# Performance work log

Measured on AMD Instinct MI355X. Metric: run time of the kernel, lower is better.

Reference implementation:

```python
import math
import jax, jax.numpy as jnp
import numpy as np

N_HEAD = 16
D_MODEL = 1024
D_K = 64
D_V = 64


def setup_inputs() -> dict:
    key = jax.random.key(0)
    ks = jax.random.split(key, 9)
    bs, s = 8, 1024
    q = jax.random.normal(ks[0], (bs, s, D_K), dtype=jnp.float32)
    k = jax.random.normal(ks[1], (bs, s, D_K), dtype=jnp.float32)
    v = jax.random.normal(ks[2], (bs, s, D_V), dtype=jnp.float32)
    # NOTE: the source module only ever uses linear_q (applied to q, k, v alike),
    # so we only materialize that projection. Torch Linear: y = x @ W.T + b.
    Wq = jax.random.normal(ks[3], (N_HEAD * D_K, D_K), dtype=jnp.float32) * 0.02
    bq = jnp.zeros((N_HEAD * D_K,), dtype=jnp.float32)
    W1 = jax.random.normal(ks[4], (D_MODEL, N_HEAD * D_V), dtype=jnp.float32) * 0.02
    b1 = jnp.zeros((D_MODEL,), dtype=jnp.float32)
    W2 = jax.random.normal(ks[5], (D_MODEL, D_MODEL), dtype=jnp.float32) * 0.02
    b2 = jnp.zeros((D_MODEL,), dtype=jnp.float32)
    return {"q": q, "k": k, "v": v, "Wq": Wq, "bq": bq,
            "W1": W1, "b1": b1, "W2": W2, "b2": b2}


def reference(q, k, v, Wq, bq, W1, b1, W2, b2):
    bs, s_q, d_k = q.shape
    h = N_HEAD
    scale = math.sqrt(d_k)
    # shared projection (source uses linear_q for all three); split heads on last dim
    proj = lambda x: (jnp.einsum('bsd,ed->bse', x, Wq) + bq).reshape(bs, -1, h, d_k)
    qh = proj(q)   # [b, s_q, h, d]
    kh = proj(k)   # [b, s_k, h, d]
    vh = proj(v)   # [b, s_v, h, d]
    e = jnp.einsum('bqhd,bkhd->bhqk', qh, kh) / scale
    a = jax.nn.softmax(e, axis=-1)  # dropout = identity in eval mode
    y = jnp.einsum('bhqk,bkhd->bqhd', a, vh).reshape(bs, s_q, h * d_k)
    # output MLP: Linear -> ReLU -> (dropout) -> Linear
    x = jax.nn.relu(jnp.einsum('bsd,ed->bse', y, W1) + b1)
    x = jnp.einsum('bsd,ed->bse', x, W2) + b2
    return x
```

## Files before the change

### kernel.cpp

```cpp
#include <hip/hip_runtime.h>
#include <math.h>

#define NB 8
#define SS 1024
#define NH 16
#define DK 64
#define EE 1024
#define DMOD 1024

using bf16x8 = __attribute__((ext_vector_type(8))) short;
using f32x4  = __attribute__((ext_vector_type(4))) float;

__device__ __forceinline__ unsigned short f2bf(float f) {
    unsigned u = __builtin_bit_cast(unsigned, f);
    u += 0x7FFFu + ((u >> 16) & 1u);
    return (unsigned short)(u >> 16);
}

__device__ __forceinline__ float exp2_hw(float x) {
#if __has_builtin(__builtin_amdgcn_exp2f)
    return __builtin_amdgcn_exp2f(x);
#else
    float r; asm("v_exp_f32 %0, %1" : "=v"(r) : "v"(x)); return r;
#endif
}

__device__ __forceinline__ unsigned cvt_pk_bf16(float lo, float hi) {
    unsigned r;
    asm("v_cvt_pk_bf16_f32 %0, %1, %2" : "=v"(r) : "v"(lo), "v"(hi));
    return r;
}

__device__ __forceinline__ void gld16(const void* g, void* l) {
    __builtin_amdgcn_global_load_lds(
        (const __attribute__((address_space(1))) void*)g,
        (__attribute__((address_space(3))) void*)l, 16, 0, 0);
}

__global__ __launch_bounds__(256) void cvt_all(
    const float* __restrict__ W1, const float* __restrict__ W2,
    const float* __restrict__ q, const float* __restrict__ k,
    const float* __restrict__ v, const float* __restrict__ Wq,
    unsigned short* __restrict__ W1b, unsigned short* __restrict__ W2b,
    unsigned short* __restrict__ qb, unsigned short* __restrict__ kb,
    unsigned short* __restrict__ vb, unsigned short* __restrict__ Wqb)
{
    const int z = blockIdx.y;
    const float* s; unsigned short* d; int n;
    switch (z) {
        case 0:  s = W1; d = W1b; n = 1048576; break;
        case 1:  s = W2; d = W2b; n = 1048576; break;
        case 2:  s = q;  d = qb;  n = 524288;  break;
        case 3:  s = k;  d = kb;  n = 524288;  break;
        case 4:  s = v;  d = vb;  n = 524288;  break;
        default: s = Wq; d = Wqb; n = 65536;   break;
    }
    const int i = (blockIdx.x * 256 + threadIdx.x) * 8;
    if (i >= n) return;
    const float4 a = *(const float4*)(s + i);
    const float4 b = *(const float4*)(s + i + 4);
    bf16x8 o;
    o[0]=(short)f2bf(a.x); o[1]=(short)f2bf(a.y); o[2]=(short)f2bf(a.z); o[3]=(short)f2bf(a.w);
    o[4]=(short)f2bf(b.x); o[5]=(short)f2bf(b.y); o[6]=(short)f2bf(b.z); o[7]=(short)f2bf(b.w);
    *(bf16x8*)(d + i) = o;
}

__global__ __launch_bounds__(256) void proj_mfma(
    const unsigned short* __restrict__ qb, const unsigned short* __restrict__ kb,
    const unsigned short* __restrict__ vb, const unsigned short* __restrict__ Wb,
    const float* __restrict__ bias, unsigned short* __restrict__ Cbase,
    float qscale)
{
    __shared__ __align__(16) unsigned short As[128 * 64];
    __shared__ __align__(16) unsigned short Bs[128 * 64];
    const int z = blockIdx.z;
    const unsigned short* X = (z == 0) ? qb : (z == 1) ? kb : vb;
    unsigned short* C = Cbase + (size_t)z * 8388608;
    const float sc = (z == 0) ? qscale : 1.0f;
    const int tid  = threadIdx.x;
    const int lane = tid & 63;
    const int w = tid >> 6, wm = w >> 1, wn = w & 1;
    const int n0 = blockIdx.x * 128, m0 = blockIdx.y * 128;
    const int lr = lane & 15, lg = lane >> 4;

    #pragma unroll
    for (int p = 0; p < 4; ++p) {
        const int c = p * 256 + tid;
        const int lb = (p * 256 + (tid & ~63)) * 8;
        gld16(X  + (size_t)m0 * DK + (size_t)c * 8, As + lb);
        gld16(Wb + (size_t)n0 * DK + (size_t)c * 8, Bs + lb);
    }
    __syncthreads();

    f32x4 acc[4][4] = {};
    #pragma unroll
    for (int kk = 0; kk < 2; ++kk) {
        bf16x8 af[4], bfr[4];
        #pragma unroll
        for (int mf = 0; mf < 4; ++mf)
            af[mf] = *(const bf16x8*)&As[(wm * 64 + mf * 16 + lr) * 64 + kk * 32 + lg * 8];
        #pragma unroll
        for (int nf = 0; nf < 4; ++nf)
            bfr[nf] = *(const bf16x8*)&Bs[(wn * 64 + nf * 16 + lr) * 64 + kk * 32 + lg * 8];
        #pragma unroll
        for (int mf = 0; mf < 4; ++mf)
            #pragma unroll
            for (int nf = 0; nf < 4; ++nf)
                acc[mf][nf] = __builtin_amdgcn_mfma_f32_16x16x32_bf16(
                    af[mf], bfr[nf], acc[mf][nf], 0, 0, 0);
    }

    #pragma unroll
    for (int nf = 0; nf < 4; ++nf) {
        const int n = n0 + wn * 64 + nf * 16 + lr;
        const float bb = bias[n];
        #pragma unroll
        for (int mf = 0; mf < 4; ++mf)
            #pragma unroll
            for (int r = 0; r < 4; ++r) {
                const int mr = m0 + wm * 64 + mf * 16 + lg * 4 + r;
                const int bh = (mr >> 10) * NH + (n >> 6);
                const int s  = mr & 1023, d = n & 63;
                const size_t idx = (z == 2)
                    ? (size_t)bh * 65536 + (size_t)d * 1024 + s
                    : (size_t)bh * 65536 + (size_t)s * 64 + d;
                C[idx] = f2bf((acc[mf][nf][r] + bb) * sc);
            }
    }
}

__global__ __launch_bounds__(256) void attn_v9(
    const unsigned short* __restrict__ Qp, const unsigned short* __restrict__ Kp,
    const unsigned short* __restrict__ Vt, unsigned short* __restrict__ Y)
{
    __shared__ __align__(16) unsigned short Ks[64 * 64];
    __shared__ __align__(16) unsigned short Vs[64 * 64];
    __shared__ __align__(16) unsigned short Ps[4][32][72];
    const int tid  = threadIdx.x;
    const int lane = tid & 63;
    const int w    = tid >> 6;
    const int flat    = blockIdx.x;
    const int logical = (flat & 7) * 128 + (flat >> 3);
    const int qt = logical & 7;
    const int bh = logical >> 3;
    const int q0 = qt * 128;
    const size_t base = (size_t)bh * (SS * DK);
    const int lr = lane & 15, lg = lane >> 4;
    const int lg4 = lg * 4;

    const int c0 = tid,       r0 = c0 >> 3, h0 = c0 & 7;
    const int c1 = 256 + tid, r1 = c1 >> 3, h1 = c1 & 7;
    const int lds0 = r0 * 64 + ((h0 ^ (r0 & 7)) << 3);
    const int lds1 = r1 * 64 + ((h1 ^ (r1 & 7)) << 3);

    const unsigned short* kbase = Kp + base;
    const unsigned short* vbase = Vt + base;
    bf16x8 kA = *(const bf16x8*)(kbase + (size_t)r0 * DK + h0 * 8);
    bf16x8 kB = *(const bf16x8*)(kbase + (size_t)r1 * DK + h1 * 8);
    bf16x8 vA = *(const bf16x8*)(vbase + (size_t)r0 * SS + h0 * 8);
    bf16x8 vB = *(const bf16x8*)(vbase + (size_t)r1 * SS + h1 * 8);
    *(bf16x8*)&Ks[lds0] = kA; *(bf16x8*)&Ks[lds1] = kB;
    *(bf16x8*)&Vs[lds0] = vA; *(bf16x8*)&Vs[lds1] = vB;

    bf16x8 bQ[2][2];
    #pragma unroll
    for (int qf = 0; qf < 2; ++qf) {
        const unsigned short* qptr =
            Qp + base + (size_t)(q0 + w * 32 + qf * 16 + lr) * DK + lg * 8;
        bQ[qf][0] = *(const bf16x8*)qptr;
        bQ[qf][1] = *(const bf16x8*)(qptr + 32);
    }

    __syncthreads();

    float m[2] = {-1e30f, -1e30f}, l[2] = {0.0f, 0.0f};
    f32x4 oacc[2][4] = {};

    for (int kt = 0; kt < 16; ++kt) {
        if (kt < 15) {
            const int s1 = (kt + 1) * 64;
            kA = *(const bf16x8*)(kbase + (size_t)(s1 + r0) * DK + h0 * 8);
            kB = *(const bf16x8*)(kbase + (size_t)(s1 + r1) * DK + h1 * 8);
            vA = *(const bf16x8*)(vbase + (size_t)r0 * SS + s1 + h0 * 8);
            vB = *(const bf16x8*)(vbase + (size_t)r1 * SS + s1 + h1 * 8);
        }

        f32x4 sacc[2][4];
        #pragma unroll
        for (int nb = 0; nb < 4; ++nb) {
            const int krow = nb * 16 + lr;
            const bf16x8 aK0 = *(const bf16x8*)&Ks[krow * 64 + ((lg       ^ (lr & 7)) << 3)];
            const bf16x8 aK1 = *(const bf16x8*)&Ks[krow * 64 + (((4 + lg) ^ (lr & 7)) << 3)];
            #pragma unroll
            for (int qf = 0; qf < 2; ++qf) {
                f32x4 z = {};
                z = __builtin_amdgcn_mfma_f32_16x16x32_bf16(aK0, bQ[qf][0], z, 0, 0, 0);
                z = __builtin_amdgcn_mfma_f32_16x16x32_bf16(aK1, bQ[qf][1], z, 0, 0, 0);
                sacc[qf][nb] = z;
            }
        }

        bf16x8 bV[2][4];
        #pragma unroll
        for (int kk = 0; kk < 2; ++kk)
            #pragma unroll
            for (int d0 = 0; d0 < 4; ++d0) {
                const int vrow = d0 * 16 + lr;
                bV[kk][d0] = *(const bf16x8*)&Vs[vrow * 64 + (((kk * 4 + lg) ^ (lr & 7)) << 3)];
            }

        #pragma unroll
        for (int qf = 0; qf < 2; ++qf) {
            float mx = sacc[qf][0][0];
            #pragma unroll
            for (int nb = 0; nb < 4; ++nb)
                #pragma unroll
                for (int r = 0; r < 4; ++r)
                    mx = fmaxf(mx, sacc[qf][nb][r]);
            mx = fmaxf(mx, __shfl_xor(mx, 16));
            mx = fmaxf(mx, __shfl_xor(mx, 32));

            if (__any(mx > m[qf] + 8.0f)) {
                const float mn = fmaxf(m[qf], mx);
                const float alpha = exp2_hw(m[qf] - mn);
                m[qf] = mn;
                l[qf] *= alpha;
                #pragma unroll
                for (int r = 0; r < 4; ++r) {
                    const float ar = __shfl(alpha, lg4 + r, 16);
                    #pragma unroll
                    for (int d0 = 0; d0 < 4; ++d0) oacc[qf][d0][r] *= ar;
                }
            }

            float p[4][4];
            float ls = 0.0f;
            #pragma unroll
            for (int nb = 0; nb < 4; ++nb)
                #pragma unroll
                for (int r = 0; r < 4; ++r) {
                    const float pv = exp2_hw(sacc[qf][nb][r] - m[qf]);
                    p[nb][r] = pv;
                    ls += pv;
                }
            ls += __shfl_xor(ls, 16);
            ls += __shfl_xor(ls, 32);
            l[qf] += ls;

            #pragma unroll
            for (int nb = 0; nb < 4; ++nb) {
                uint2 pw;
                pw.x = cvt_pk_bf16(p[nb][0], p[nb][1]);
                pw.y = cvt_pk_bf16(p[nb][2], p[nb][3]);
                *(uint2*)&Ps[w][qf * 16 + lr][nb * 16 + lg4] = pw;
            }

            #pragma unroll
            for (int kk = 0; kk < 2; ++kk) {
                const bf16x8 aP = *(const bf16x8*)&Ps[w][qf * 16 + lr][kk * 32 + lg * 8];
                #pragma unroll
                for (int d0 = 0; d0 < 4; ++d0)
                    oacc[qf][d0] = __builtin_amdgcn_mfma_f32_16x16x32_bf16(
                        aP, bV[kk][d0], oacc[qf][d0], 0, 0, 0);
            }
        }

        if (kt < 15) {
            __syncthreads();
            *(bf16x8*)&Ks[lds0] = kA; *(bf16x8*)&Ks[lds1] = kB;
            *(bf16x8*)&Vs[lds0] = vA; *(bf16x8*)&Vs[lds1] = vB;
            __syncthreads();
        }
    }

    const int hh = bh & 15, bb = bh >> 4;
    #pragma unroll
    for (int qf = 0; qf < 2; ++qf) {
        const float linv = 1.0f / l[qf];
        #pragma unroll
        for (int r = 0; r < 4; ++r) {
            const float lri = __shfl(linv, lg4 + r, 16);
            const int qr = q0 + w * 32 + qf * 16 + lg4 + r;
            unsigned short* dst = Y + (size_t)(bb * SS + qr) * EE + hh * DK;
            #pragma unroll
            for (int d0 = 0; d0 < 4; ++d0)
                dst[d0 * 16 + lr] = f2bf(oacc[qf][d0][r] * lri);
        }
    }
}

template<bool RELU, bool OUT_BF16>
__global__ __launch_bounds__(256) void mlp_gemm(
    const unsigned short* __restrict__ A, const unsigned short* __restrict__ B,
    const float* __restrict__ bias, void* __restrict__ Cv)
{
    constexpr int K = 1024, N = 1024;
    __shared__ __align__(16) unsigned short As[128 * 64];
    __shared__ __align__(16) unsigned short Bs[128 * 64];
    const int tid  = threadIdx.x;
    const int lane = tid & 63;
    const int w = tid >> 6, wm = w >> 1, wn = w & 1;
    const int flat    = blockIdx.x;
    const int logical = (flat & 7) * 64 + (flat >> 3);
    const int n0 = (logical & 7) * 128, m0 = (logical >> 3) * 128;
    const int lr = lane & 15, lg = lane >> 4;

    f32x4 acc[4][4] = {};

    for (int kt = 0; kt < K; kt += 64) {
        __syncthreads();
        #pragma unroll
        for (int p = 0; p < 4; ++p) {
            const int c = p * 256 + tid;
            const int row = c >> 3, col = (c & 7) * 8;
            const int lb = (p * 256 + (tid & ~63)) * 8;
            gld16(A + (size_t)(m0 + row) * K + kt + col, As + lb);
            gld16(B + (size_t)(n0 + row) * K + kt + col, Bs + lb);
        }
        __syncthreads();
        #pragma unroll
        for (int kk = 0; kk < 2; ++kk) {
            bf16x8 af[4], bfr[4];
            #pragma unroll
            for (int mf = 0; mf < 4; ++mf)
                af[mf] = *(const bf16x8*)&As[(wm * 64 + mf * 16 + lr) * 64 + kk * 32 + lg * 8];
            #pragma unroll
            for (int nf = 0; nf < 4; ++nf)
                bfr[nf] = *(const bf16x8*)&Bs[(wn * 64 + nf * 16 + lr) * 64 + kk * 32 + lg * 8];
            #pragma unroll
            for (int mf = 0; mf < 4; ++mf)
                #pragma unroll
                for (int nf = 0; nf < 4; ++nf)
                    acc[mf][nf] = __builtin_amdgcn_mfma_f32_16x16x32_bf16(
                        af[mf], bfr[nf], acc[mf][nf], 0, 0, 0);
        }
    }

    #pragma unroll
    for (int nf = 0; nf < 4; ++nf) {
        const int cc = n0 + wn * 64 + nf * 16 + lr;
        const float bb = bias[cc];
        #pragma unroll
        for (int mf = 0; mf < 4; ++mf) {
            #pragma unroll
            for (int r = 0; r < 4; ++r) {
                float x = acc[mf][nf][r] + bb;
                if (RELU) x = fmaxf(x, 0.0f);
                const size_t rr = (size_t)(m0 + wm * 64 + mf * 16 + lg * 4 + r);
                if (OUT_BF16) ((unsigned short*)Cv)[rr * N + cc] = f2bf(x);
                else          ((float*)Cv)[rr * N + cc] = x;
            }
        }
    }
}

extern "C" void kernel_launch(void* const* d_in, const int* in_sizes, int n_in,
                              void* d_out, int out_size, void* d_ws, size_t ws_size,
                              hipStream_t stream) {
    const float* q  = (const float*)d_in[0];
    const float* k  = (const float*)d_in[1];
    const float* v  = (const float*)d_in[2];
    const float* Wq = (const float*)d_in[3];
    const float* bq = (const float*)d_in[4];
    const float* W1 = (const float*)d_in[5];
    const float* b1 = (const float*)d_in[6];
    const float* W2 = (const float*)d_in[7];
    const float* b2 = (const float*)d_in[8];

    unsigned short* wsu = (unsigned short*)d_ws;
    unsigned short* Qp  = wsu;
    unsigned short* Kp  = wsu + (size_t)8388608;
    unsigned short* Vt  = wsu + (size_t)16777216;
    unsigned short* Y   = wsu + (size_t)25165824;
    unsigned short* W1b = wsu + (size_t)33554432;
    unsigned short* W2b = wsu + (size_t)34603008;
    unsigned short* qb  = wsu + (size_t)35651584;
    unsigned short* kb  = wsu + (size_t)36175872;
    unsigned short* vb  = wsu + (size_t)36700160;
    unsigned short* Wqb = wsu + (size_t)37224448;
    unsigned short* H1  = Qp;

    dim3 blk(256);

    cvt_all<<<dim3(512, 6), blk, 0, stream>>>(W1, W2, q, k, v, Wq,
                                              W1b, W2b, qb, kb, vb, Wqb);

    const float qscale = 0.125f * 1.44269504088896340736f;
    proj_mfma<<<dim3(8, 64, 3), blk, 0, stream>>>(qb, kb, vb, Wqb, bq, Qp, qscale);

    attn_v9<<<1024, blk, 0, stream>>>(Qp, Kp, Vt, Y);

    mlp_gemm<true,  true ><<<512, blk, 0, stream>>>(Y,  W1b, b1, H1);
    mlp_gemm<false, false><<<512, blk, 0, stream>>>(H1, W2b, b2, d_out);
}
```

Measured before the change: 152.8 us.

## Fuse input bf16 conversion into projection, stage epilogue via LDS, double K/V tile

The fp32-to-bf16 conversion of q, k, v moves out of the standalone convert kernel and into the projection GEMM's tile load. This removes a bf16 round trip through global memory. The projection epilogue now writes results to LDS, transposed for V, and then emits 16-byte coalesced stores instead of scattered 2-byte writes. The attention kernel now processes two 64-key subtiles per outer iteration, which halves the number of barrier-synchronized LDS refills at the cost of more LDS and registers.

Result: slower. 159.4 us (+4.4%).

```diff
diff --git a/kernel.cpp b/kernel.cpp
--- a/kernel.cpp
+++ b/kernel.cpp
@@ -37,22 +37,17 @@
         (__attribute__((address_space(3))) void*)l, 16, 0, 0);
 }
 
-__global__ __launch_bounds__(256) void cvt_all(
+__global__ __launch_bounds__(256) void cvt_w(
     const float* __restrict__ W1, const float* __restrict__ W2,
-    const float* __restrict__ q, const float* __restrict__ k,
-    const float* __restrict__ v, const float* __restrict__ Wq,
+    const float* __restrict__ Wq,
     unsigned short* __restrict__ W1b, unsigned short* __restrict__ W2b,
-    unsigned short* __restrict__ qb, unsigned short* __restrict__ kb,
-    unsigned short* __restrict__ vb, unsigned short* __restrict__ Wqb)
+    unsigned short* __restrict__ Wqb)
 {
     const int z = blockIdx.y;
     const float* s; unsigned short* d; int n;
     switch (z) {
         case 0:  s = W1; d = W1b; n = 1048576; break;
         case 1:  s = W2; d = W2b; n = 1048576; break;
-        case 2:  s = q;  d = qb;  n = 524288;  break;
-        case 3:  s = k;  d = kb;  n = 524288;  break;
-        case 4:  s = v;  d = vb;  n = 524288;  break;
         default: s = Wq; d = Wqb; n = 65536;   break;
     }
     const int i = (blockIdx.x * 256 + threadIdx.x) * 8;
@@ -65,16 +60,18 @@
     *(bf16x8*)(d + i) = o;
 }
 
+#define OTP 136
 __global__ __launch_bounds__(256) void proj_mfma(
-    const unsigned short* __restrict__ qb, const unsigned short* __restrict__ kb,
-    const unsigned short* __restrict__ vb, const unsigned short* __restrict__ Wb,
+    const float* __restrict__ qf32, const float* __restrict__ kf32,
+    const float* __restrict__ vf32, const unsigned short* __restrict__ Wb,
     const float* __restrict__ bias, unsigned short* __restrict__ Cbase,
     float qscale)
 {
-    __shared__ __align__(16) unsigned short As[128 * 64];
-    __shared__ __align__(16) unsigned short Bs[128 * 64];
+    __shared__ __align__(16) unsigned short Sh[128 * OTP];
+    unsigned short* As = Sh;
+    unsigned short* Bs = Sh + 8192;
     const int z = blockIdx.z;
-    const unsigned short* X = (z == 0) ? qb : (z == 1) ? kb : vb;
+    const float* X = (z == 0) ? qf32 : (z == 1) ? kf32 : vf32;
     unsigned short* C = Cbase + (size_t)z * 8388608;
     const float sc = (z == 0) ? qscale : 1.0f;
     const int tid  = threadIdx.x;
@@ -86,9 +83,15 @@
     #pragma unroll
     for (int p = 0; p < 4; ++p) {
         const int c = p * 256 + tid;
+        const int row = c >> 3, col = (c & 7) * 8;
         const int lb = (p * 256 + (tid & ~63)) * 8;
-        gld16(X  + (size_t)m0 * DK + (size_t)c * 8, As + lb);
         gld16(Wb + (size_t)n0 * DK + (size_t)c * 8, Bs + lb);
+        const float4 a = *(const float4*)(X + (size_t)(m0 + row) * DK + col);
+        const float4 b = *(const float4*)(X + (size_t)(m0 + row) * DK + col + 4);
+        bf16x8 o;
+        o[0]=(short)f2bf(a.x); o[1]=(short)f2bf(a.y); o[2]=(short)f2bf(a.z); o[3]=(short)f2bf(a.w);
+        o[4]=(short)f2bf(b.x); o[5]=(short)f2bf(b.y); o[6]=(short)f2bf(b.z); o[7]=(short)f2bf(b.w);
+        *(bf16x8*)&As[row * 64 + col] = o;
     }
     __syncthreads();
 
@@ -110,31 +113,48 @@
                     af[mf], bfr[nf], acc[mf][nf], 0, 0, 0);
     }
 
+    __syncthreads();
+
     #pragma unroll
     for (int nf = 0; nf < 4; ++nf) {
-        const int n = n0 + wn * 64 + nf * 16 + lr;
-        const float bb = bias[n];
+        const int nl = wn * 64 + nf * 16 + lr;
+        const float bb = bias[n0 + nl];
         #pragma unroll
         for (int mf = 0; mf < 4; ++mf)
             #pragma unroll
             for (int r = 0; r < 4; ++r) {
-                const int mr = m0 + wm * 64 + mf * 16 + lg * 4 + r;
-                const int bh = (mr >> 10) * NH + (n >> 6);
-                const int s  = mr & 1023, d = n & 63;
-                const size_t idx = (z == 2)
-                    ? (size_t)bh * 65536 + (size_t)d * 1024 + s
-                    : (size_t)bh * 65536 + (size_t)s * 64 + d;
-                C[idx] = f2bf((acc[mf][nf][r] + bb) * sc);
-            }
-    }
-}
-
-__global__ __launch_bounds__(256) void attn_v9(
+                const int ml = wm * 64 + mf * 16 + lg * 4 + r;
+                const unsigned short v = f2bf((acc[mf][nf][r] + bb) * sc);
+                if (z == 2) Sh[nl * OTP + ml] = v;
+                else        Sh[ml * OTP + nl] = v;
+            }
+    }
+    __syncthreads();
+
+    const int row = tid >> 1, half = tid & 1;
+    unsigned short* dst;
+    if (z == 2) {
+        const int n = n0 + row;
+        const int bh = (m0 >> 10) * NH + (n >> 6);
+        dst = C + (size_t)bh * 65536 + (size_t)(n & 63) * 1024
+                + (m0 & 1023) + half * 64;
+    } else {
+        const int mr = m0 + row;
+        const int bh = (mr >> 10) * NH + ((n0 + half * 64) >> 6);
+        dst = C + (size_t)bh * 65536 + (size_t)(mr & 1023) * 64;
+    }
+    const unsigned short* srcr = &Sh[row * OTP + half * 64];
+    #pragma unroll
+    for (int j = 0; j < 8; ++j)
+        *(bf16x8*)(dst + j * 8) = *(const bf16x8*)(srcr + j * 8);
+}
+
+__global__ __launch_bounds__(256) void attn_v10(
     const unsigned short* __restrict__ Qp, const unsigned short* __restrict__ Kp,
     const unsigned short* __restrict__ Vt, unsigned short* __restrict__ Y)
 {
-    __shared__ __align__(16) unsigned short Ks[64 * 64];
-    __shared__ __align__(16) unsigned short Vs[64 * 64];
+    __shared__ __align__(16) unsigned short Ks[2][64 * 64];
+    __shared__ __align__(16) unsigned short Vs[2][64 * 64];
     __shared__ __align__(16) unsigned short Ps[4][32][72];
     const int tid  = threadIdx.x;
     const int lane = tid & 63;
@@ -155,12 +175,15 @@
 
     const unsigned short* kbase = Kp + base;
     const unsigned short* vbase = Vt + base;
-    bf16x8 kA = *(const bf16x8*)(kbase + (size_t)r0 * DK + h0 * 8);
-    bf16x8 kB = *(const bf16x8*)(kbase + (size_t)r1 * DK + h1 * 8);
-    bf16x8 vA = *(const bf16x8*)(vbase + (size_t)r0 * SS + h0 * 8);
-    bf16x8 vB = *(const bf16x8*)(vbase + (size_t)r1 * SS + h1 * 8);
-    *(bf16x8*)&Ks[lds0] = kA; *(bf16x8*)&Ks[lds1] = kB;
-    *(bf16x8*)&Vs[lds0] = vA; *(bf16x8*)&Vs[lds1] = vB;
+
+    #pragma unroll
+    for (int sub = 0; sub < 2; ++sub) {
+        const int sb = sub * 64;
+        *(bf16x8*)&Ks[sub][lds0] = *(const bf16x8*)(kbase + (size_t)(sb + r0) * DK + h0 * 8);
+        *(bf16x8*)&Ks[sub][lds1] = *(const bf16x8*)(kbase + (size_t)(sb + r1) * DK + h1 * 8);
+        *(bf16x8*)&Vs[sub][lds0] = *(const bf16x8*)(vbase + (size_t)r0 * SS + sb + h0 * 8);
+        *(bf16x8*)&Vs[sub][lds1] = *(const bf16x8*)(vbase + (size_t)r1 * SS + sb + h1 * 8);
+    }
 
     bf16x8 bQ[2][2];
     #pragma unroll
@@ -175,100 +198,110 @@
 
     float m[2] = {-1e30f, -1e30f}, l[2] = {0.0f, 0.0f};
     f32x4 oacc[2][4] = {};
-
-    for (int kt = 0; kt < 16; ++kt) {
-        if (kt < 15) {
-            const int s1 = (kt + 1) * 64;
-            kA = *(const bf16x8*)(kbase + (size_t)(s1 + r0) * DK + h0 * 8);
-            kB = *(const bf16x8*)(kbase + (size_t)(s1 + r1) * DK + h1 * 8);
-            vA = *(const bf16x8*)(vbase + (size_t)r0 * SS + s1 + h0 * 8);
-            vB = *(const bf16x8*)(vbase + (size_t)r1 * SS + s1 + h1 * 8);
-        }
-
-        f32x4 sacc[2][4];
-        #pragma unroll
-        for (int nb = 0; nb < 4; ++nb) {
-            const int krow = nb * 16 + lr;
-            const bf16x8 aK0 = *(const bf16x8*)&Ks[krow * 64 + ((lg       ^ (lr & 7)) << 3)];
-            const bf16x8 aK1 = *(const bf16x8*)&Ks[krow * 64 + (((4 + lg) ^ (lr & 7)) << 3)];
+    bf16x8 kPA[2], kPB[2], vPA[2], vPB[2];
+
+    for (int kt = 0; kt < 8; ++kt) {
+        if (kt < 7) {
+            #pragma unroll
+            for (int sub = 0; sub < 2; ++sub) {
+                const int sb = (kt + 1) * 128 + sub * 64;
+                kPA[sub] = *(const bf16x8*)(kbase + (size_t)(sb + r0) * DK + h0 * 8);
+                kPB[sub] = *(const bf16x8*)(kbase + (size_t)(sb + r1) * DK + h1 * 8);
+                vPA[sub] = *(const bf16x8*)(vbase + (size_t)r0 * SS + sb + h0 * 8);
+                vPB[sub] = *(const bf16x8*)(vbase + (size_t)r1 * SS + sb + h1 * 8);
+            }
+        }
+
+        #pragma unroll
+        for (int sub = 0; sub < 2; ++sub) {
+            f32x4 sacc[2][4];
+            #pragma unroll
+            for (int nb = 0; nb < 4; ++nb) {
+                const int krow = nb * 16 + lr;
+                const bf16x8 aK0 = *(const bf16x8*)&Ks[sub][krow * 64 + ((lg       ^ (lr & 7)) << 3)];
+                const bf16x8 aK1 = *(const bf16x8*)&Ks[sub][krow * 64 + (((4 + lg) ^ (lr & 7)) << 3)];
+                #pragma unroll
+                for (int qf = 0; qf < 2; ++qf) {
+                    f32x4 z = {};
+                    z = __builtin_amdgcn_mfma_f32_16x16x32_bf16(aK0, bQ[qf][0], z, 0, 0, 0);
+                    z = __builtin_amdgcn_mfma_f32_16x16x32_bf16(aK1, bQ[qf][1], z, 0, 0, 0);
+                    sacc[qf][nb] = z;
+                }
+            }
+
+            bf16x8 bV[2][4];
+            #pragma unroll
+            for (int kk = 0; kk < 2; ++kk)
+                #pragma unroll
+                for (int d0 = 0; d0 < 4; ++d0) {
+                    const int vrow = d0 * 16 + lr;
+                    bV[kk][d0] = *(const bf16x8*)&Vs[sub][vrow * 64 + (((kk * 4 + lg) ^ (lr & 7)) << 3)];
+                }
+
             #pragma unroll
             for (int qf = 0; qf < 2; ++qf) {
-                f32x4 z = {};
-                z = __builtin_amdgcn_mfma_f32_16x16x32_bf16(aK0, bQ[qf][0], z, 0, 0, 0);
-                z = __builtin_amdgcn_mfma_f32_16x16x32_bf16(aK1, bQ[qf][1], z, 0, 0, 0);
-                sacc[qf][nb] = z;
-            }
-        }
-
-        bf16x8 bV[2][4];
-        #pragma unroll
-        for (int kk = 0; kk < 2; ++kk)
-            #pragma unroll
-            for (int d0 = 0; d0 < 4; ++d0) {
-                const int vrow = d0 * 16 + lr;
-                bV[kk][d0] = *(const bf16x8*)&Vs[vrow * 64 + (((kk * 4 + lg) ^ (lr & 7)) << 3)];
-            }
-
-        #pragma unroll
-        for (int qf = 0; qf < 2; ++qf) {
-            float mx = sacc[qf][0][0];
-            #pragma unroll
-            for (int nb = 0; nb < 4; ++nb)
-                #pragma unroll
-                for (int r = 0; r < 4; ++r)
-                    mx = fmaxf(mx, sacc[qf][nb][r]);
-            mx = fmaxf(mx, __shfl_xor(mx, 16));
-            mx = fmaxf(mx, __shfl_xor(mx, 32));
-
-            if (__any(mx > m[qf] + 8.0f)) {
-                const float mn = fmaxf(m[qf], mx);
-                const float alpha = exp2_hw(m[qf] - mn);
-                m[qf] = mn;
-                l[qf] *= alpha;
-                #pragma unroll
-                for (int r = 0; r < 4; ++r) {
-                    const float ar = __shfl(alpha, lg4 + r, 16);
+                float mx = sacc[qf][0][0];
+                #pragma unroll
+                for (int nb = 0; nb < 4; ++nb)
                     #pragma unroll
-                    for (int d0 = 0; d0 < 4; ++d0) oacc[qf][d0][r] *= ar;
+                    for (int r = 0; r < 4; ++r)
+                        mx = fmaxf(mx, sacc[qf][nb][r]);
+                mx = fmaxf(mx, __shfl_xor(mx, 16));
+                mx = fmaxf(mx, __shfl_xor(mx, 32));
+
+                if (__any(mx > m[qf] + 8.0f)) {
+                    const float mn = fmaxf(m[qf], mx);
+                    const float alpha = exp2_hw(m[qf] - mn);
+                    m[qf] = mn;
+                    l[qf] *= alpha;
+                    #pragma unroll
+                    for (int r = 0; r < 4; ++r) {
+                        const float ar = __shfl(alpha, lg4 + r, 16);
+                        #pragma unroll
+                        for (int d0 = 0; d0 < 4; ++d0) oacc[qf][d0][r] *= ar;
+                    }
                 }
-            }
-
-            float p[4][4];
-            float ls = 0.0f;
-            #pragma unroll
-            for (int nb = 0; nb < 4; ++nb)
-                #pragma unroll
-                for (int r = 0; r < 4; ++r) {
-                    const float pv = exp2_hw(sacc[qf][nb][r] - m[qf]);
-                    p[nb][r] = pv;
-                    ls += pv;
+
+                float p[4][4];
+                float ls = 0.0f;
+                #pragma unroll
+                for (int nb = 0; nb < 4; ++nb)
+                    #pragma unroll
+                    for (int r = 0; r < 4; ++r) {
+                        const float pv = exp2_hw(sacc[qf][nb][r] - m[qf]);
+                        p[nb][r] = pv;
+                        ls += pv;
+                    }
+                ls += __shfl_xor(ls, 16);
+                ls += __shfl_xor(ls, 32);
+                l[qf] += ls;
+
+                #pragma unroll
+                for (int nb = 0; nb < 4; ++nb) {
+                    uint2 pw;
+                    pw.x = cvt_pk_bf16(p[nb][0], p[nb][1]);
+                    pw.y = cvt_pk_bf16(p[nb][2], p[nb][3]);
+                    *(uint2*)&Ps[w][qf * 16 + lr][nb * 16 + lg4] = pw;
                 }
-            ls += __shfl_xor(ls, 16);
-            ls += __shfl_xor(ls, 32);
-            l[qf] += ls;
-
-            #pragma unroll
-            for (int nb = 0; nb < 4; ++nb) {
-                uint2 pw;
-                pw.x = cvt_pk_bf16(p[nb][0], p[nb][1]);
-                pw.y = cvt_pk_bf16(p[nb][2], p[nb][3]);
-                *(uint2*)&Ps[w][qf * 16 + lr][nb * 16 + lg4] = pw;
-            }
-
-            #pragma unroll
-            for (int kk = 0; kk < 2; ++kk) {
-                const bf16x8 aP = *(const bf16x8*)&Ps[w][qf * 16 + lr][kk * 32 + lg * 8];
-                #pragma unroll
-                for (int d0 = 0; d0 < 4; ++d0)
-                    oacc[qf][d0] = __builtin_amdgcn_mfma_f32_16x16x32_bf16(
-                        aP, bV[kk][d0], oacc[qf][d0], 0, 0, 0);
-            }
-        }
-
-        if (kt < 15) {
+
+                #pragma unroll
+                for (int kk = 0; kk < 2; ++kk) {
+                    const bf16x8 aP = *(const bf16x8*)&Ps[w][qf * 16 + lr][kk * 32 + lg * 8];
+                    #pragma unroll
+                    for (int d0 = 0; d0 < 4; ++d0)
+                        oacc[qf][d0] = __builtin_amdgcn_mfma_f32_16x16x32_bf16(
+                            aP, bV[kk][d0], oacc[qf][d0], 0, 0, 0);
+                }
+            }
+        }
+
+        if (kt < 7) {
             __syncthreads();
-            *(bf16x8*)&Ks[lds0] = kA; *(bf16x8*)&Ks[lds1] = kB;
-            *(bf16x8*)&Vs[lds0] = vA; *(bf16x8*)&Vs[lds1] = vB;
+            #pragma unroll
+            for (int sub = 0; sub < 2; ++sub) {
+                *(bf16x8*)&Ks[sub][lds0] = kPA[sub]; *(bf16x8*)&Ks[sub][lds1] = kPB[sub];
+                *(bf16x8*)&Vs[sub][lds0] = vPA[sub]; *(bf16x8*)&Vs[sub][lds1] = vPB[sub];
+            }
             __syncthreads();
         }
     }
@@ -374,21 +407,17 @@
     unsigned short* Y   = wsu + (size_t)25165824;
     unsigned short* W1b = wsu + (size_t)33554432;
     unsigned short* W2b = wsu + (size_t)34603008;
-    unsigned short* qb  = wsu + (size_t)35651584;
-    unsigned short* kb  = wsu + (size_t)36175872;
-    unsigned short* vb  = wsu + (size_t)36700160;
-    unsigned short* Wqb = wsu + (size_t)37224448;
+    unsigned short* Wqb = wsu + (size_t)35651584;
     unsigned short* H1  = Qp;
 
     dim3 blk(256);
 
-    cvt_all<<<dim3(512, 6), blk, 0, stream>>>(W1, W2, q, k, v, Wq,
-                                              W1b, W2b, qb, kb, vb, Wqb);
+    cvt_w<<<dim3(512, 3), blk, 0, stream>>>(W1, W2, Wq, W1b, W2b, Wqb);
 
     const float qscale = 0.125f * 1.44269504088896340736f;
-    proj_mfma<<<dim3(8, 64, 3), blk, 0, stream>>>(qb, kb, vb, Wqb, bq, Qp, qscale);
-
-    attn_v9<<<1024, blk, 0, stream>>>(Qp, Kp, Vt, Y);
+    proj_mfma<<<dim3(8, 64, 3), blk, 0, stream>>>(q, k, v, Wqb, bq, Qp, qscale);
+
+    attn_v10<<<1024, blk, 0, stream>>>(Qp, Kp, Vt, Y);
 
     mlp_gemm<true,  true ><<<512, blk, 0, stream>>>(Y,  W1b, b1, H1);
     mlp_gemm<false, false><<<512, blk, 0, stream>>>(H1, W2b, b2, d_out);
```
